# Kernel tuning notes

Measured on AMD Instinct MI355X. Metric: run time of the kernel, lower is better.

Reference implementation:

```python
import jax, jax.numpy as jnp
import numpy as np
from jax import lax

B, N, C = 2, 4096, 8
MAX_DET = 100
SCORE_THR = 0.01
NMS_THR = 0.5
NEG = -1e30  # sentinel for masked scores


def setup_inputs() -> dict:
    key = jax.random.key(0)
    k1, k2, k3, k4, k5 = jax.random.split(key, 5)
    # valid xyxy boxes: centers in [0,512), extents in [2,66)
    ctr = jax.random.uniform(k1, (B, N, 2), dtype=jnp.float32) * 512.0
    wh = jax.random.uniform(k2, (B, N, 2), dtype=jnp.float32) * 64.0 + 2.0
    boxes = jnp.concatenate([ctr - wh / 2, ctr + wh / 2], axis=-1)  # [B,N,4]
    classification = jax.random.uniform(k3, (B, N, C), dtype=jnp.float32)
    rotation = jax.random.normal(k4, (B, N, 3), dtype=jnp.float32)
    translation = jax.random.normal(k5, (B, N, 3), dtype=jnp.float32)
    return {"boxes": boxes, "classification": classification,
            "rotation": rotation, "translation": translation}


def _pairwise_iou(b):
    # b: [N,4] xyxy, torchvision convention (no +1)
    x1, y1, x2, y2 = b[:, 0], b[:, 1], b[:, 2], b[:, 3]
    area = (x2 - x1) * (y2 - y1)
    ix1 = jnp.maximum(x1[:, None], x1[None, :])
    iy1 = jnp.maximum(y1[:, None], y1[None, :])
    ix2 = jnp.minimum(x2[:, None], x2[None, :])
    iy2 = jnp.minimum(y2[:, None], y2[None, :])
    inter = jnp.clip(ix2 - ix1, 0.0) * jnp.clip(iy2 - iy1, 0.0)
    union = area[:, None] + area[None, :] - inter
    return inter / jnp.maximum(union, 1e-9)


def _nms_keep(boxes, scores, valid):
    # greedy NMS matching torchvision.ops.nms on the `valid` subset.
    order = jnp.argsort(-jnp.where(valid, scores, NEG))  # score-descending
    iou = _pairwise_iou(boxes[order])  # [N,N]
    idx = jnp.arange(N)
    keep0 = valid[order]

    def body(i, keep):
        sup = keep[i] & (iou[i] > NMS_THR) & (idx > i)
        return keep & ~sup

    keep_sorted = lax.fori_loop(0, N, body, keep0)
    return jnp.zeros(N, bool).at[order].set(keep_sorted)


def _filter_image(boxes, cls, rot, trans):
    # boxes [N,4], cls [N,C], rot [N,3], trans [N,3]
    def per_class(scores):
        valid = scores > SCORE_THR
        keep = _nms_keep(boxes, scores, valid)
        return jnp.where(keep, scores, NEG)

    masked = jax.vmap(per_class, in_axes=1)(cls)  # [C,N]
    topv, topi = lax.top_k(masked.reshape(-1), MAX_DET)
    labels = topi // N
    anchors = topi % N
    ok = topv > NEG / 2
    okc = ok[:, None]
    boxes_o = jnp.where(okc, boxes[anchors], -1.0)
    scores_o = jnp.where(ok, topv, -1.0)
    labels_o = jnp.where(ok, labels, -1)
    rot_o = jnp.where(okc, rot[anchors], -1.0)
    trans_o = jnp.where(okc, trans[anchors], -1.0)
    return boxes_o, scores_o, labels_o, rot_o, trans_o


def reference(boxes, classification, rotation, translation):
    return jax.vmap(_filter_image)(boxes, classification, rotation, translation)
```

## Files before the change

### kernel.cpp

```cpp
#include <hip/hip_runtime.h>
#include <stdint.h>

#define B_ 2
#define N_ 4096
#define C_ 8
#define MAXDET 100
#define SCORE_THR 0.01f
#define NMS_THR 0.5f
#define NEGV -1e30f

typedef unsigned long long u64;

__device__ __forceinline__ unsigned mono_key(float f) {
    unsigned u = __float_as_uint(f);
    return (u & 0x80000000u) ? ~u : (u | 0x80000000u);
}
__device__ __forceinline__ float mono_dec(unsigned m) {
    return (m & 0x80000000u) ? __uint_as_float(m ^ 0x80000000u)
                             : __uint_as_float(~m);
}
__device__ __forceinline__ bool iou_gt_half(float inter, float uni) {
    return (inter + inter - uni) > uni * 0x1p-25f;
}
__device__ __forceinline__ void wave_fence() {
    asm volatile("s_waitcnt lgkmcnt(0)" ::: "memory");
}

__device__ __forceinline__ void ce_shfl(u64 &e0, u64 &e1, int tid, int size,
                                        int stride, bool desc) {
    const int m = stride >> 1;
    bool d = (((2 * tid) & size) == 0) ? desc : !desc;
    bool lower = (tid & m) == 0;
    u64 p0 = __shfl_xor(e0, m, 64);
    u64 p1 = __shfl_xor(e1, m, 64);
    bool takeMax = (d == lower);
    e0 = takeMax ? (e0 > p0 ? e0 : p0) : (e0 < p0 ? e0 : p0);
    e1 = takeMax ? (e1 > p1 ? e1 : p1) : (e1 < p1 ? e1 : p1);
}
__device__ __forceinline__ void ce_intra(u64 &e0, u64 &e1, int tid, int size,
                                         bool desc) {
    bool d = (((2 * tid) & size) == 0) ? desc : !desc;
    if ((e0 < e1) == d) { u64 t = e0; e0 = e1; e1 = t; }
}
__device__ __forceinline__ void bitonic_reg128(u64 &e0, u64 &e1, int tid,
                                               bool desc) {
    #pragma unroll
    for (int size = 2; size <= 128; size <<= 1) {
        #pragma unroll
        for (int stride = size >> 1; stride >= 2; stride >>= 1)
            ce_shfl(e0, e1, tid, size, stride, desc);
        ce_intra(e0, e1, tid, size, desc);
    }
}
__device__ __forceinline__ void merge_hybrid(u64 &e0, u64 &e1, u64* k, int tid,
                                             int size, bool desc) {
    k[2 * tid] = e0; k[2 * tid + 1] = e1;
    __syncthreads();
    for (int stride = size >> 1; stride >= 128; stride >>= 1) {
        int pos = 2 * tid - (tid & (stride - 1));
        int par = pos + stride;
        bool d = ((pos & size) == 0) ? desc : !desc;
        u64 a = k[pos], bb = k[par];
        if ((a < bb) == d) { k[pos] = bb; k[par] = a; }
        __syncthreads();
    }
    e0 = k[2 * tid]; e1 = k[2 * tid + 1];
    #pragma unroll
    for (int stride = 64; stride >= 2; stride >>= 1)
        ce_shfl(e0, e1, tid, size, stride, desc);
    ce_intra(e0, e1, tid, size, desc);
}

__global__ __launch_bounds__(512) void mega_kernel(
    const float* __restrict__ cls,
    const float* __restrict__ boxes,
    const float* __restrict__ rot,
    const float* __restrict__ trans,
    u64* __restrict__ cand,
    int* __restrict__ cnt,
    float* __restrict__ out)
{
    __shared__ u64 m[4096];
    __shared__ u64 scr[1024];
    __shared__ float4 sb192[192];
    __shared__ float  sa192[192];
    __shared__ u64 cm[576];
    __shared__ float4 sbx[64];
    __shared__ u64 shJ[64];
    __shared__ int s_fin;
    __shared__ int s_elect;

    const int bc = blockIdx.x;
    const int b = bc >> 3, cls_id = bc & 7;
    const int tid = threadIdx.x;
    const int lane = tid & 63;
    const int wave = tid >> 6;
    const float4* boxes4 = (const float4*)boxes;

    float sreg[8];
    #pragma unroll
    for (int q = 0; q < 4; q++) {
        int i0 = q * 1024 + 2 * tid;
        sreg[2 * q]     = cls[((size_t)b * N_ + i0) * C_ + cls_id];
        sreg[2 * q + 1] = cls[((size_t)b * N_ + i0 + 1) * C_ + cls_id];
    }

    #pragma unroll 1
    for (int q = 0; q < 4; q++) {
        const bool desc = ((q & 1) == 0);
        int i0 = q * 1024 + 2 * tid;
        float f0 = (sreg[2 * q]     > SCORE_THR) ? sreg[2 * q]     : NEGV;
        float f1 = (sreg[2 * q + 1] > SCORE_THR) ? sreg[2 * q + 1] : NEGV;
        u64 e0 = ((u64)mono_key(f0) << 32) | (unsigned)(~i0);
        u64 e1 = ((u64)mono_key(f1) << 32) | (unsigned)(~(i0 + 1));
        u64* k = &m[q * 1024];
        bitonic_reg128(e0, e1, tid, desc);
        merge_hybrid(e0, e1, k, tid, 256, desc);
        merge_hybrid(e0, e1, k, tid, 512, desc);
        merge_hybrid(e0, e1, k, tid, 1024, desc);
        k[2 * tid] = e0; k[2 * tid + 1] = e1;
        __syncthreads();
    }

    {
        u64 e0, e1;
        int i = 2 * tid;
        int qq = i >> 8;
        int off = qq * 1024 + ((qq & 1) ? 768 : 0) + (i & 255);
        e0 = m[off]; e1 = m[off + 1];
        merge_hybrid(e0, e1, scr, tid, 512, true);
        merge_hybrid(e0, e1, scr, tid, 1024, true);
        scr[2 * tid] = e0; scr[2 * tid + 1] = e1;
    }
    __syncthreads();

    if (tid < 192) {
        int orig = (int)(~(unsigned)scr[tid]);
        float4 bx = boxes4[(size_t)b * N_ + orig];
        sb192[tid] = bx;
        sa192[tid] = (bx.z - bx.x) * (bx.w - bx.y);
    }
    __syncthreads();

    for (int qq = tid; qq < 576; qq += 512) {
        int r = qq / 3, w = qq - 3 * r;
        int chunk = r >> 6;
        u64 bits = 0ull;
        if (w >= chunk) {
            float4 bi = sb192[r];
            float aarea = sa192[r];
            #pragma unroll 8
            for (int t = 0; t < 64; t++) {
                float4 bj = sb192[w * 64 + t];
                float barea = sa192[w * 64 + t];
                float ix1 = fmaxf(bi.x, bj.x);
                float iy1 = fmaxf(bi.y, bj.y);
                float ix2 = fminf(bi.z, bj.z);
                float iy2 = fminf(bi.w, bj.w);
                float inter = fmaxf(ix2 - ix1, 0.0f) * fmaxf(iy2 - iy1, 0.0f);
                float uni = fmaxf(aarea + barea - inter, 1e-9f);
                if (iou_gt_half(inter, uni)) bits |= (1ull << t);
            }
            if (w == chunk) bits &= ~((2ull << (r & 63)) - 1ull);
        }
        cm[qq] = bits;
    }
    __syncthreads();

    if (wave == 0) {
        u64 remv = 0ull;
        int cc = 0;
        bool fin = false;
        for (int c = 0; c < 3; c++) {
            int p = c * 64 + lane;
            u64 key = scr[p];
            float sc = mono_dec((unsigned)(key >> 32));
            u64 validb = __ballot(sc > -1e29f);
            if (validb == 0ull) { fin = true; break; }

            u64 curw = __shfl(remv, c, 64);
            u64 kept = 0ull;
            for (int t = 0; t < 64; t++) {
                u64 iv = cm[(c * 64 + t) * 3 + c];
                u64 bit = 1ull << t;
                if (!(curw & bit) && (validb & bit)) { kept |= bit; curw |= iv; }
            }

            if ((kept >> lane) & 1ull) {
                int rank = cc + __popcll(kept & ((1ull << lane) - 1ull));
                if (rank < 128) {
                    int orig = (int)(~(unsigned)key);
                    unsigned flat = (unsigned)(cls_id * N_ + orig);
                    cand[bc * 128 + rank] =
                        ((u64)mono_key(sc) << 32) | (unsigned)(~flat);
                }
            }
            cc += __popcll(kept);
            if (cc >= 128) { fin = true; break; }

            if (lane < 3) {
                u64 acc = 0ull;
                for (int t = 0; t < 64; t++)
                    if ((kept >> t) & 1ull) acc |= cm[(c * 64 + t) * 3 + lane];
                remv |= acc;
            }
        }
        if (fin) {
            int filled = cc < 128 ? cc : 128;
            for (int s = lane; s < 128; s += 64)
                if (s >= filled) cand[bc * 128 + s] = 0ull;
        }
        if (lane == 0) s_fin = fin ? 1 : 0;
    }
    __syncthreads();

    if (!s_fin) {
        for (int size = 2048; size <= 4096; size <<= 1) {
            for (int stride = size >> 1; stride > 0; stride >>= 1) {
                for (int t = tid; t < 2048; t += 512) {
                    int pos = 2 * t - (t & (stride - 1));
                    int par = pos + stride;
                    bool d = ((pos & size) == 0);
                    u64 a = m[pos], bb = m[par];
                    if ((a < bb) == d) { m[pos] = bb; m[par] = a; }
                }
                __syncthreads();
            }
        }
        if (wave == 0) {
            u64 remv = 0ull;
            int cc = 0;
            for (int c = 0; c < 64; c++) {
                int p = c * 64 + lane;
                u64 key = m[p];
                float sc = mono_dec((unsigned)(key >> 32));
                u64 validb = __ballot(sc > -1e29f);
                if (validb == 0ull) break;

                int orig = (int)(~(unsigned)key);
                float4 bl = boxes4[(size_t)b * N_ + orig];
                sbx[lane] = bl;
                wave_fence();
                float al = (bl.z - bl.x) * (bl.w - bl.y);

                u64 intra = 0ull;
                for (int t = 0; t < 64; t++) {
                    float4 bj = sbx[t];
                    float ab = (bj.z - bj.x) * (bj.w - bj.y);
                    float ix1 = fmaxf(bl.x, bj.x);
                    float iy1 = fmaxf(bl.y, bj.y);
                    float ix2 = fminf(bl.z, bj.z);
                    float iy2 = fminf(bl.w, bj.w);
                    float inter = fmaxf(ix2 - ix1, 0.0f) * fmaxf(iy2 - iy1, 0.0f);
                    float uni = fmaxf(al + ab - inter, 1e-9f);
                    if (t > lane && iou_gt_half(inter, uni)) intra |= (1ull << t);
                }
                shJ[lane] = intra;
                wave_fence();

                u64 curw = __shfl(remv, c, 64);
                u64 kept = 0ull;
                for (int t = 0; t < 64; t++) {
                    u64 iv = shJ[t];
                    u64 bit = 1ull << t;
                    if (!(curw & bit) && (validb & bit)) { kept |= bit; curw |= iv; }
                }

                if ((kept >> lane) & 1ull) {
                    int rank = cc + __popcll(kept & ((1ull << lane) - 1ull));
                    if (rank < 128) {
                        unsigned flat = (unsigned)(cls_id * N_ + orig);
                        cand[bc * 128 + rank] =
                            ((u64)mono_key(sc) << 32) | (unsigned)(~flat);
                    }
                }
                cc += __popcll(kept);
                if (cc >= 128) break;

                if (lane > c) {
                    u64 accw = 0ull;
                    for (int u = 0; u < 64; u++) {
                        int pj = lane * 64 + u;
                        int oj = (int)(~(unsigned)m[pj]);
                        float4 bj = boxes4[(size_t)b * N_ + oj];
                        float ab = (bj.z - bj.x) * (bj.w - bj.y);
                        bool sup = false;
                        for (int tt = 0; tt < 64; tt++) {
                            if (!((kept >> tt) & 1ull)) continue;
                            float4 br = sbx[tt];
                            float ar = (br.z - br.x) * (br.w - br.y);
                            float ix1 = fmaxf(br.x, bj.x);
                            float iy1 = fmaxf(br.y, bj.y);
                            float ix2 = fminf(br.z, bj.z);
                            float iy2 = fminf(br.w, bj.w);
                            float inter = fmaxf(ix2 - ix1, 0.0f) * fmaxf(iy2 - iy1, 0.0f);
                            float uni = fmaxf(ar + ab - inter, 1e-9f);
                            if (iou_gt_half(inter, uni)) { sup = true; break; }
                        }
                        if (sup) accw |= (1ull << u);
                    }
                    remv |= accw;
                }
                wave_fence();
            }
            int filled = cc < 128 ? cc : 128;
            for (int s = lane; s < 128; s += 64)
                if (s >= filled) cand[bc * 128 + s] = 0ull;
        }
        __syncthreads();
    }

    __threadfence();
    if (tid == 0) {
        int old = atomicAdd(&cnt[b], 1);
        s_elect = (old == 7) ? 1 : 0;
    }
    __syncthreads();
    if (!s_elect) return;
    __threadfence();

    {
        const u64* candb = cand + (size_t)b * 1024;
        int i = 2 * tid;
        int c8 = i >> 7;
        int ss = i & 127;
        u64 f0, f1;
        if (c8 & 1) {
            f0 = candb[c8 * 128 + 127 - ss];
            f1 = candb[c8 * 128 + 126 - ss];
        } else {
            f0 = candb[i];
            f1 = candb[i + 1];
        }
        merge_hybrid(f0, f1, scr, tid, 256, true);
        merge_hybrid(f0, f1, scr, tid, 512, true);
        merge_hybrid(f0, f1, scr, tid, 1024, true);
        scr[2 * tid] = f0; scr[2 * tid + 1] = f1;
        __syncthreads();

        if (tid < MAXDET) {
            u64 key = scr[tid];
            float score = mono_dec((unsigned)(key >> 32));
            bool ok = score > (NEGV * 0.5f);
            unsigned flat = (~(unsigned)key) & 32767u;
            int cc8 = flat >> 12;
            int n = flat & (N_ - 1);

            float* obox = out;
            float* oscr = out + 800;
            float* olab = out + 1000;
            float* orot = out + 1200;
            float* otrn = out + 1800;

            #pragma unroll
            for (int d = 0; d < 4; d++)
                obox[b * 400 + tid * 4 + d] =
                    ok ? boxes[((size_t)b * N_ + n) * 4 + d] : -1.0f;
            oscr[b * MAXDET + tid] = ok ? score : -1.0f;
            olab[b * MAXDET + tid] = ok ? (float)cc8 : -1.0f;
            #pragma unroll
            for (int d = 0; d < 3; d++) {
                orot[b * 300 + tid * 3 + d] =
                    ok ? rot[((size_t)b * N_ + n) * 3 + d] : -1.0f;
                otrn[b * 300 + tid * 3 + d] =
                    ok ? trans[((size_t)b * N_ + n) * 3 + d] : -1.0f;
            }
        }
    }
}

extern "C" void kernel_launch(void* const* d_in, const int* in_sizes, int n_in,
                              void* d_out, int out_size, void* d_ws, size_t ws_size,
                              hipStream_t stream) {
    const float* boxes = (const float*)d_in[0];
    const float* cls   = (const float*)d_in[1];
    const float* rot   = (const float*)d_in[2];
    const float* trans = (const float*)d_in[3];
    float* out = (float*)d_out;

    char* w = (char*)d_ws;
    u64* cand = (u64*)w;
    int* cnt  = (int*)(w + 16384);

    hipMemsetAsync(cnt, 0, 2 * sizeof(int), stream);
    mega_kernel<<<B_ * C_, 512, 0, stream>>>(cls, boxes, rot, trans,
                                             cand, cnt, out);
}
```

Measured before the change: 119.2 us.

## Split per-class chunk sorting across four blocks with atomic last-block election

The four 1024-element sort chunks per (batch, class) are now handled by four separate blocks, launching 64 blocks instead of 16. Each block writes its sorted chunk to a global keys buffer, and the last block to finish (chosen by an atomic counter) carries on with the merge, NMS and final top-k stages. This adds parallelism to the sort phase, which was serial before, at the cost of a global round trip for the keys and an extra counter handshake. The fallback path now reloads the full key array from global memory.

Result: no change. 119.2 us (+0.0%).

```diff
diff --git a/kernel.cpp b/kernel.cpp
--- a/kernel.cpp
+++ b/kernel.cpp
@@ -71,13 +71,15 @@
     ce_intra(e0, e1, tid, size, desc);
 }
 
-__global__ __launch_bounds__(512) void mega_kernel(
+__global__ __launch_bounds__(512) void mega2_kernel(
     const float* __restrict__ cls,
     const float* __restrict__ boxes,
     const float* __restrict__ rot,
     const float* __restrict__ trans,
+    u64* __restrict__ keys,
     u64* __restrict__ cand,
-    int* __restrict__ cnt,
+    int* __restrict__ cnt1,
+    int* __restrict__ cnt2,
     float* __restrict__ out)
 {
     __shared__ u64 m[4096];
@@ -90,44 +92,50 @@
     __shared__ int s_fin;
     __shared__ int s_elect;
 
-    const int bc = blockIdx.x;
+    const int g = blockIdx.x;
+    const int q = g & 3;
+    const int bc = g >> 2;
     const int b = bc >> 3, cls_id = bc & 7;
     const int tid = threadIdx.x;
     const int lane = tid & 63;
     const int wave = tid >> 6;
+    const size_t kbase = (size_t)bc * N_;
     const float4* boxes4 = (const float4*)boxes;
 
-    float sreg[8];
-    #pragma unroll
-    for (int q = 0; q < 4; q++) {
-        int i0 = q * 1024 + 2 * tid;
-        sreg[2 * q]     = cls[((size_t)b * N_ + i0) * C_ + cls_id];
-        sreg[2 * q + 1] = cls[((size_t)b * N_ + i0 + 1) * C_ + cls_id];
-    }
-
-    #pragma unroll 1
-    for (int q = 0; q < 4; q++) {
+    {
         const bool desc = ((q & 1) == 0);
         int i0 = q * 1024 + 2 * tid;
-        float f0 = (sreg[2 * q]     > SCORE_THR) ? sreg[2 * q]     : NEGV;
-        float f1 = (sreg[2 * q + 1] > SCORE_THR) ? sreg[2 * q + 1] : NEGV;
+        float s0 = cls[((size_t)b * N_ + i0) * C_ + cls_id];
+        float s1 = cls[((size_t)b * N_ + i0 + 1) * C_ + cls_id];
+        float f0 = (s0 > SCORE_THR) ? s0 : NEGV;
+        float f1 = (s1 > SCORE_THR) ? s1 : NEGV;
         u64 e0 = ((u64)mono_key(f0) << 32) | (unsigned)(~i0);
         u64 e1 = ((u64)mono_key(f1) << 32) | (unsigned)(~(i0 + 1));
-        u64* k = &m[q * 1024];
         bitonic_reg128(e0, e1, tid, desc);
-        merge_hybrid(e0, e1, k, tid, 256, desc);
-        merge_hybrid(e0, e1, k, tid, 512, desc);
-        merge_hybrid(e0, e1, k, tid, 1024, desc);
-        k[2 * tid] = e0; k[2 * tid + 1] = e1;
-        __syncthreads();
-    }
+        merge_hybrid(e0, e1, scr, tid, 256, desc);
+        merge_hybrid(e0, e1, scr, tid, 512, desc);
+        merge_hybrid(e0, e1, scr, tid, 1024, desc);
+        ulonglong2 v; v.x = e0; v.y = e1;
+        *(ulonglong2*)&keys[kbase + q * 1024 + 2 * tid] = v;
+    }
+
+    __syncthreads();
+    __threadfence();
+    if (tid == 0) {
+        int old = atomicAdd(&cnt1[bc], 1);
+        s_elect = (old == 3) ? 1 : 0;
+    }
+    __syncthreads();
+    if (!s_elect) return;
+    __threadfence();
 
     {
         u64 e0, e1;
         int i = 2 * tid;
         int qq = i >> 8;
         int off = qq * 1024 + ((qq & 1) ? 768 : 0) + (i & 255);
-        e0 = m[off]; e1 = m[off + 1];
+        ulonglong2 v = *(const ulonglong2*)&keys[kbase + off];
+        e0 = v.x; e1 = v.y;
         merge_hybrid(e0, e1, scr, tid, 512, true);
         merge_hybrid(e0, e1, scr, tid, 1024, true);
         scr[2 * tid] = e0; scr[2 * tid + 1] = e1;
@@ -215,6 +223,8 @@
     __syncthreads();
 
     if (!s_fin) {
+        for (int i = tid; i < 4096; i += 512) m[i] = keys[kbase + i];
+        __syncthreads();
         for (int size = 2048; size <= 4096; size <<= 1) {
             for (int stride = size >> 1; stride > 0; stride >>= 1) {
                 for (int t = tid; t < 2048; t += 512) {
@@ -312,7 +322,7 @@
 
     __threadfence();
     if (tid == 0) {
-        int old = atomicAdd(&cnt[b], 1);
+        int old = atomicAdd(&cnt2[b], 1);
         s_elect = (old == 7) ? 1 : 0;
     }
     __syncthreads();
@@ -379,10 +389,12 @@
     float* out = (float*)d_out;
 
     char* w = (char*)d_ws;
-    u64* cand = (u64*)w;
-    int* cnt  = (int*)(w + 16384);
-
-    hipMemsetAsync(cnt, 0, 2 * sizeof(int), stream);
-    mega_kernel<<<B_ * C_, 512, 0, stream>>>(cls, boxes, rot, trans,
-                                             cand, cnt, out);
-}
+    u64* keys = (u64*)w;
+    u64* cand = (u64*)(w + 524288);
+    int* cnt  = (int*)(w + 524288 + 16384);
+
+    hipMemsetAsync(cnt, 0, 18 * sizeof(int), stream);
+    mega2_kernel<<<B_ * C_ * 4, 512, 0, stream>>>(cls, boxes, rot, trans,
+                                                  keys, cand, cnt, cnt + 16,
+                                                  out);
+}
```
